# Kernel optimization log

Measured on AMD Instinct MI355X. Metric: run time of the kernel, lower is better.

Reference implementation:

```python
import jax, jax.numpy as jnp
import numpy as np
from jax import lax

HIDDEN = 1024
OUT = 768  # g_gpt_emb_dim (distilgpt2 n_embd)
BATCH = 512


def setup_inputs() -> dict:
    key = jax.random.key(0)
    ks = jax.random.split(key, 8)
    s_i = 1.0 / np.sqrt(HIDDEN)
    return {
        "src": jax.random.normal(ks[0], (1, BATCH, OUT), jnp.float32),
        "hidden": jax.random.normal(ks[1], (1, BATCH, HIDDEN), jnp.float32),
        "W_ih": jax.random.uniform(ks[2], (3 * HIDDEN, OUT), jnp.float32, -s_i, s_i),
        "W_hh": jax.random.uniform(ks[3], (3 * HIDDEN, HIDDEN), jnp.float32, -s_i, s_i),
        "b_ih": jax.random.uniform(ks[4], (3 * HIDDEN,), jnp.float32, -s_i, s_i),
        "b_hh": jax.random.uniform(ks[5], (3 * HIDDEN,), jnp.float32, -s_i, s_i),
        "fc_W": jax.random.uniform(ks[6], (OUT, 2 * HIDDEN), jnp.float32, -s_i, s_i),
        "fc_b": jax.random.uniform(ks[7], (OUT,), jnp.float32, -s_i, s_i),
        "output_len": 256,
    }


def reference(src, hidden, W_ih, W_hh, b_ih, b_hh, fc_W, fc_b, output_len):
    # src: [src_len, B, OUT]; hidden: [1, B, H]
    context = hidden[0]          # [B, H] (kept fixed across steps)
    h0 = hidden[0]               # [B, H] GRU state
    x0 = src[0]                  # [B, OUT] first decoder input

    def gru_cell(x, h):
        # PyTorch GRU cell: gates ordered (r, z, n)
        gi = x @ W_ih.T + b_ih   # [B, 3H]
        gh = h @ W_hh.T + b_hh   # [B, 3H]
        i_r, i_z, i_n = jnp.split(gi, 3, axis=-1)
        h_r, h_z, h_n = jnp.split(gh, 3, axis=-1)
        r = jax.nn.sigmoid(i_r + h_r)
        z = jax.nn.sigmoid(i_z + h_z)
        n = jnp.tanh(i_n + r * h_n)
        return (1.0 - z) * n + z * h

    def step(carry, _):
        h, x = carry
        h_new = gru_cell(x, h)                                   # [B, H]
        emb_con = jnp.concatenate([h_new, context], axis=-1)     # [B, 2H]
        fc_out = emb_con @ fc_W.T + fc_b                         # [B, OUT]
        return (h_new, fc_out), fc_out

    _, outputs = lax.scan(step, (h0, x0), None, length=output_len)
    return outputs  # [output_len, B, OUT]
```

## Files before the change

kernel.cpp:

```cpp
#include <hip/hip_runtime.h>

#define H    1024
#define OUTD 768
#define BSZ  512
#define TSTEPS 256
#define N3H  3072
#define NEXT 4864
#define TILE_E 4096
#define MT_E   65536
#define SLOT_E 524288

typedef __attribute__((ext_vector_type(8))) short bf16x8;
typedef __attribute__((ext_vector_type(4))) float f32x4;

__device__ __forceinline__ unsigned short f2bf(float f){
  unsigned u = __builtin_bit_cast(unsigned, f);
  u += 0x7fffu + ((u >> 16) & 1u);
  return (unsigned short)(u >> 16);
}
__device__ __forceinline__ float sigm(float x){ return 1.f/(1.f+__expf(-x)); }

__device__ __forceinline__ int swz_off(int r, int c){
  return (r<<6) | (((c>>3) ^ (r&7))<<3) | (c&7);
}

#define GLOAD16(gp, lp) __builtin_amdgcn_global_load_lds( \
    (__attribute__((address_space(1))) void*)(gp), \
    (__attribute__((address_space(3))) void*)(lp), 16, 0, 0)

__global__ void conv_bf(unsigned short* dst, const float* src, int n){
  int i = blockIdx.x*256 + threadIdx.x;
  if (i < n) dst[i] = f2bf(src[i]);
}
__global__ void conv_rows(unsigned short* dst, const float* src, int rows, int cols,
                          int sstride, int soff){
  int i = blockIdx.x*256 + threadIdx.x;
  if (i < rows*cols){ int r = i/cols, c = i - r*cols; dst[i] = f2bf(src[r*sstride + soff + c]); }
}
__global__ void transp_fcw(unsigned short* dst, const float* fcw){
  __shared__ float tile[64][65];
  int k0 = blockIdx.x*64, o0 = blockIdx.y*64;
  int t = threadIdx.x; int rr = t>>2, cs = (t&3)*16;
  for (int j=0;j<16;j++) tile[rr][cs+j] = fcw[(size_t)(o0+rr)*2048 + k0+cs+j];
  __syncthreads();
  for (int j=0;j<16;j++) dst[(size_t)(k0+rr)*768 + o0+cs+j] = f2bf(tile[cs+j][rr]);
}

__global__ void asm_wext(unsigned short* Wext, const float* Wcomb, const float* Whh,
                         const float* fcW){
  int idx = blockIdx.x*256 + threadIdx.x;
  if (idx >= NEXT*H) return;
  int n = idx >> 10, k = idx & 1023;
  float v;
  if (n < 4096){
    int c = (n>>4)&3, jj = ((n>>6)<<4) | (n&15);
    if (c==0)      v = Wcomb[(size_t)jj*H + k]       + Whh[(size_t)jj*H + k];
    else if (c==1) v = Wcomb[(size_t)(H+jj)*H + k]   + Whh[(size_t)(H+jj)*H + k];
    else if (c==2) v = Wcomb[(size_t)(2*H+jj)*H + k];
    else           v = Whh[(size_t)(2*H+jj)*H + k];
  } else {
    v = fcW[(size_t)(n-4096)*2048 + k];
  }
  Wext[(size_t)(n>>6)*MT_E + (k>>6)*TILE_E + swz_off(n&63, k&63)] = f2bf(v);
}

__global__ void asm_const(float* cst, const float* dmat, const float* fcctx,
                          const float* b_hh){
  int idx = blockIdx.x*256 + threadIdx.x;
  if (idx >= BSZ*NEXT) return;
  int b = idx / NEXT, n = idx - b*NEXT;
  float v;
  if (n < 4096){
    int c = (n>>4)&3, jj = ((n>>6)<<4) | (n&15);
    if (c==0)      v = dmat[(size_t)b*N3H + jj]       + b_hh[jj];
    else if (c==1) v = dmat[(size_t)b*N3H + H + jj]   + b_hh[H+jj];
    else if (c==2) v = dmat[(size_t)b*N3H + 2*H + jj];
    else           v = b_hh[2*H + jj];
  } else {
    v = fcctx[(size_t)b*OUTD + (n-4096)];
  }
  cst[idx] = v;
}

__global__ void gru0(const float* gi, const float* gh, const float* hidden,
                     unsigned short* hbf, float* hf){
  int idx = blockIdx.x*256 + threadIdx.x;
  if (idx >= BSZ*H) return;
  int b = idx >> 10, j = idx & 1023;
  float r  = sigm(gi[(size_t)b*N3H + j]       + gh[(size_t)b*N3H + j]);
  float z  = sigm(gi[(size_t)b*N3H + H + j]   + gh[(size_t)b*N3H + H + j]);
  float nn = tanhf(gi[(size_t)b*N3H + 2*H + j] + r*gh[(size_t)b*N3H + 2*H + j]);
  float ho = hidden[idx];
  float hn = nn + z*(ho - nn);
  hf[idx] = hn;
  hbf[(size_t)(b>>6)*MT_E + (j>>6)*TILE_E + swz_off(b&63, j&63)] = f2bf(hn);
}

__global__ __launch_bounds__(256) void gemm_bt(const unsigned short* __restrict__ A,
    const unsigned short* __restrict__ Bt, const float* __restrict__ bias,
    float* __restrict__ C, int N, int K){
  __shared__ unsigned short As[64][72];
  __shared__ unsigned short Bs[64][72];
  int tid = threadIdx.x, wave = tid>>6, lane = tid&63;
  int m0 = blockIdx.y*64, n0 = blockIdx.x*64;
  int lr = tid>>2, lc = (tid&3)*16;
  const unsigned short* Ag = A + (size_t)(m0+lr)*K + lc;
  const unsigned short* Bg = Bt + (size_t)(n0+lr)*K + lc;
  f32x4 acc[4];
  #pragma unroll
  for (int c=0;c<4;c++) acc[c] = (f32x4)0.f;
  int arow = wave*16 + (lane&15);
  int koff = (lane>>4)*8;
  for (int k0=0;k0<K;k0+=64){
    *(uint4*)&As[lr][lc]   = *(const uint4*)(Ag + k0);
    *(uint4*)&As[lr][lc+8] = *(const uint4*)(Ag + k0 + 8);
    *(uint4*)&Bs[lr][lc]   = *(const uint4*)(Bg + k0);
    *(uint4*)&Bs[lr][lc+8] = *(const uint4*)(Bg + k0 + 8);
    __syncthreads();
    #pragma unroll
    for (int kk=0;kk<2;kk++){
      bf16x8 af = *(const bf16x8*)&As[arow][kk*32 + koff];
      #pragma unroll
      for (int c=0;c<4;c++){
        bf16x8 bfr = *(const bf16x8*)&Bs[c*16 + (lane&15)][kk*32 + koff];
        acc[c] = __builtin_amdgcn_mfma_f32_16x16x32_bf16(af, bfr, acc[c], 0, 0, 0);
      }
    }
    __syncthreads();
  }
  int col = lane&15, rbase = m0 + wave*16 + (lane>>4)*4;
  #pragma unroll
  for (int c=0;c<4;c++){
    int n = n0 + c*16 + col;
    float bv = bias ? bias[n] : 0.f;
    #pragma unroll
    for (int i=0;i<4;i++) C[(size_t)(rbase+i)*N + n] = acc[c][i] + bv;
  }
}

__device__ __forceinline__ void mm64(const unsigned short* __restrict__ At,
                                     const unsigned short* __restrict__ Bt,
                                     unsigned short* sA, unsigned short* sB,
                                     f32x4 acc[4]){
  const int tid = threadIdx.x, wave = tid>>6, lane = tid&63;
  const int l8 = lane>>4, lx = lane&7;
  const int xg = ((l8 ^ lx) << 3);
  const int offA = ((wave<<4) | (lane&15))*64 + xg;
  const int offB = (lane&15)*64 + xg;
  const unsigned short* ga = At + (wave<<9) + (lane<<3);
  const unsigned short* gb = Bt + (wave<<9) + (lane<<3);
  unsigned short* lA = sA + (wave<<9);
  unsigned short* lB = sB + (wave<<9);
  GLOAD16(ga, lA); GLOAD16(ga+2048, lA+2048);
  GLOAD16(gb, lB); GLOAD16(gb+2048, lB+2048);
  __syncthreads();
  #pragma unroll 2
  for (int kt=0; kt<16; kt++){
    const int cb = kt & 1;
    if (kt < 15){
      const unsigned short* gan = ga + (kt+1)*TILE_E;
      const unsigned short* gbn = gb + (kt+1)*TILE_E;
      const int bo = (cb^1) << 12;
      GLOAD16(gan, lA+bo); GLOAD16(gan+2048, lA+bo+2048);
      GLOAD16(gbn, lB+bo); GLOAD16(gbn+2048, lB+bo+2048);
    }
    const unsigned short* A0 = sA + (cb<<12);
    const unsigned short* B0 = sB + (cb<<12);
    #pragma unroll
    for (int kk=0; kk<2; kk++){
      bf16x8 av = *(const bf16x8*)(A0 + (offA ^ (kk<<5)));
      #pragma unroll
      for (int c=0; c<4; c++){
        bf16x8 bv = *(const bf16x8*)(B0 + ((offB + (c<<10)) ^ (kk<<5)));
        acc[c] = __builtin_amdgcn_mfma_f32_16x16x32_bf16(av, bv, acc[c], 0, 0, 0);
      }
    }
    __syncthreads();
  }
}

__global__ __launch_bounds__(256) void gemm_rec(const unsigned short* __restrict__ hin,
    const float* __restrict__ hfin, const unsigned short* __restrict__ Wext,
    const float* __restrict__ cst, float* __restrict__ outp,
    unsigned short* __restrict__ hout, float* __restrict__ hfout){
  __shared__ __align__(16) unsigned short sA[2*4096];
  __shared__ __align__(16) unsigned short sB[2*4096];
  const int gx = gridDim.x;
  const int f = blockIdx.x + gx*blockIdx.y;
  const int q = f & 7, mm = f >> 3;
  const int v = q*gx + mm;
  const int bx = v >> 3, by = v & 7;
  f32x4 acc[4];
  #pragma unroll
  for (int c=0;c<4;c++) acc[c] = (f32x4)0.f;
  mm64(hin + (size_t)by*MT_E, Wext + (size_t)bx*MT_E, sA, sB, acc);
  const int tid = threadIdx.x, wave = tid>>6, lane = tid&63;
  const int col = lane & 15;
  const int rbase = by*64 + wave*16 + (lane>>4)*4;
  if (bx < 64){
    const int jj = bx*16 + col;
    const float* cbp = cst + bx*64 + col;
    const int tb = (jj>>6)*TILE_E;
    #pragma unroll
    for (int i=0;i<4;i++){
      const int b = rbase + i;
      const float* cr = cbp + (size_t)b*NEXT;
      float r  = sigm(acc[0][i] + cr[0]);
      float z  = sigm(acc[1][i] + cr[16]);
      float nn = tanhf((acc[2][i] + cr[32]) + r*(acc[3][i] + cr[48]));
      float hn = nn + z*(hfin[(size_t)b*H + jj] - nn);
      hfout[(size_t)b*H + jj] = hn;
      hout[(size_t)(b>>6)*MT_E + tb + swz_off(b&63, jj&63)] = f2bf(hn);
    }
  } else {
    const int o0 = (bx-64)*64;
    #pragma unroll
    for (int c=0;c<4;c++){
      const int oc = o0 + c*16 + col;
      #pragma unroll
      for (int i=0;i<4;i++){
        const int b = rbase + i;
        outp[(size_t)b*OUTD + oc] = acc[c][i] + cst[(size_t)b*NEXT + 4096 + oc];
      }
    }
  }
}

__global__ __launch_bounds__(256) void gemm_out(const unsigned short* __restrict__ hist,
    const unsigned short* __restrict__ Wext, const float* __restrict__ fcctx,
    float* __restrict__ outp){
  __shared__ __align__(16) unsigned short sA[2*4096];
  __shared__ __align__(16) unsigned short sB[2*4096];
  const int bx = blockIdx.x;
  const int g  = blockIdx.y;
  f32x4 acc[4];
  #pragma unroll
  for (int c=0;c<4;c++) acc[c] = (f32x4)0.f;
  mm64(hist + (size_t)g*MT_E, Wext + (size_t)(64+bx)*MT_E, sA, sB, acc);
  const int tid = threadIdx.x, wave = tid>>6, lane = tid&63;
  const int col = lane & 15;
  const int s = g>>3, mb = g&7;
  const int rb = mb*64 + wave*16 + (lane>>4)*4;
  float* outs = outp + (size_t)s*BSZ*OUTD;
  #pragma unroll
  for (int c=0;c<4;c++){
    const int oc = bx*64 + c*16 + col;
    #pragma unroll
    for (int i=0;i<4;i++){
      const int b = rb + i;
      outs[(size_t)b*OUTD + oc] = acc[c][i] + fcctx[(size_t)b*OUTD + oc];
    }
  }
}

extern "C" void kernel_launch(void* const* d_in, const int* in_sizes, int n_in,
                              void* d_out, int out_size, void* d_ws, size_t ws_size,
                              hipStream_t stream){
  const float* src    = (const float*)d_in[0];
  const float* hidden = (const float*)d_in[1];
  const float* W_ih   = (const float*)d_in[2];
  const float* W_hh   = (const float*)d_in[3];
  const float* b_ih   = (const float*)d_in[4];
  const float* b_hh   = (const float*)d_in[5];
  const float* fc_W   = (const float*)d_in[6];
  const float* fc_b   = (const float*)d_in[7];
  float* outp = (float*)d_out;

  char* p = (char*)d_ws;
  auto alloc = [&](size_t bytes){ char* r = p; p += (bytes + 255) & ~(size_t)255; return r; };
  unsigned short* Wih_bf   = (unsigned short*)alloc((size_t)N3H*OUTD*2);
  unsigned short* Whh_bf   = (unsigned short*)alloc((size_t)N3H*H*2);
  unsigned short* fcWbt    = (unsigned short*)alloc((size_t)OUTD*H*2);
  unsigned short* fcWT     = (unsigned short*)alloc((size_t)H*OUTD*2);
  unsigned short* ctx_bf   = (unsigned short*)alloc((size_t)BSZ*H*2);
  unsigned short* x0_bf    = (unsigned short*)alloc((size_t)BSZ*OUTD*2);
  float*          fcctx    = (float*)alloc((size_t)BSZ*OUTD*4);
  unsigned short* fcctx_bf = (unsigned short*)alloc((size_t)BSZ*OUTD*2);
  float*          Wcomb    = (float*)alloc((size_t)N3H*H*4);
  float*          dmat     = (float*)alloc((size_t)BSZ*N3H*4);
  unsigned short* Wext     = (unsigned short*)alloc((size_t)NEXT*H*2);
  float*          cst      = (float*)alloc((size_t)BSZ*NEXT*4);
  float*          gi       = (float*)alloc((size_t)BSZ*N3H*4);
  float*          gh       = (float*)alloc((size_t)BSZ*N3H*4);
  unsigned short* hbf      = (unsigned short*)alloc((size_t)2*BSZ*H*2);
  float*          hf       = (float*)alloc((size_t)2*BSZ*H*4);

  size_t used = (size_t)(p - (char*)d_ws);
  size_t hist_bytes = (size_t)TSTEPS*BSZ*H*2;
  bool defer = (used + hist_bytes + 4096) <= ws_size;
  unsigned short* hist = defer ? (unsigned short*)alloc(hist_bytes) : nullptr;

  auto cdiv = [](int a, int b){ return (a + b - 1)/b; };

  conv_bf<<<cdiv(N3H*OUTD,256),256,0,stream>>>(Wih_bf, W_ih, N3H*OUTD);
  conv_bf<<<cdiv(N3H*H,256),256,0,stream>>>(Whh_bf, W_hh, N3H*H);
  conv_bf<<<cdiv(BSZ*H,256),256,0,stream>>>(ctx_bf, hidden, BSZ*H);
  conv_bf<<<cdiv(BSZ*OUTD,256),256,0,stream>>>(x0_bf, src, BSZ*OUTD);
  conv_rows<<<cdiv(OUTD*H,256),256,0,stream>>>(fcWbt, fc_W, OUTD, H, 2*H, H);
  transp_fcw<<<dim3(16,12),256,0,stream>>>(fcWT, fc_W);

  gemm_bt<<<dim3(H/64, N3H/64),256,0,stream>>>(Wih_bf, fcWT, nullptr, Wcomb, H, OUTD);
  gemm_bt<<<dim3(OUTD/64, BSZ/64),256,0,stream>>>(ctx_bf, fcWbt, fc_b, fcctx, OUTD, H);
  conv_bf<<<cdiv(BSZ*OUTD,256),256,0,stream>>>(fcctx_bf, fcctx, BSZ*OUTD);
  gemm_bt<<<dim3(N3H/64, BSZ/64),256,0,stream>>>(fcctx_bf, Wih_bf, b_ih, dmat, N3H, OUTD);

  asm_wext<<<cdiv(NEXT*H,256),256,0,stream>>>(Wext, Wcomb, W_hh, fc_W);
  asm_const<<<cdiv(BSZ*NEXT,256),256,0,stream>>>(cst, dmat, fcctx, b_hh);

  gemm_bt<<<dim3(N3H/64, BSZ/64),256,0,stream>>>(x0_bf, Wih_bf, b_ih, gi, N3H, OUTD);
  gemm_bt<<<dim3(N3H/64, BSZ/64),256,0,stream>>>(ctx_bf, Whh_bf, b_hh, gh, N3H, H);

  if (defer){
    gru0<<<cdiv(BSZ*H,256),256,0,stream>>>(gi, gh, hidden, hist, hf + SLOT_E);
    for (int t=1; t<TSTEPS; t++){
      gemm_rec<<<dim3(64,8),256,0,stream>>>(
          hist + (size_t)(t-1)*SLOT_E, hf + (size_t)(t&1)*SLOT_E,
          Wext, cst, nullptr,
          hist + (size_t)t*SLOT_E, hf + (size_t)((t+1)&1)*SLOT_E);
    }
    gemm_out<<<dim3(12,2048),256,0,stream>>>(hist, Wext, fcctx, outp);
  } else {
    gru0<<<cdiv(BSZ*H,256),256,0,stream>>>(gi, gh, hidden, hbf + SLOT_E, hf + SLOT_E);
    for (int t=1; t<=TSTEPS; t++){
      gemm_rec<<<dim3(76,8),256,0,stream>>>(
          hbf + (size_t)(t&1)*SLOT_E, hf + (size_t)(t&1)*SLOT_E,
          Wext, cst, outp + (size_t)(t-1)*BSZ*OUTD,
          hbf + (size_t)((t+1)&1)*SLOT_E, hf + (size_t)((t+1)&1)*SLOT_E);
    }
  }
}
```

Baseline: 4.287 ms.

## Generalize MFMA GEMM core to larger register-blocked tiles with explicit waitcnt pipelining

Replaces the fixed 64x64 mm64 routine with a templated mmcore that gives each wave a 2x4 fragment block, so A fragments are reused across more MFMAs. The recurrent GEMM now covers 64x128 tiles with half the blocks, and the output GEMM uses 128x128 tiles with 512 threads. Staging is now two tiles ahead, governed by explicit s_waitcnt vmcnt and raw barriers in place of __syncthreads. This cuts LDS traffic per MFMA and barrier overhead. The cost is fewer blocks per recurrent step, meaning less parallelism across CUs, and more register pressure.

Result: faster. 3.839 ms (-10.5%).

```diff
diff --git a/kernel.cpp b/kernel.cpp
--- a/kernel.cpp
+++ b/kernel.cpp
@@ -27,6 +27,17 @@
 #define GLOAD16(gp, lp) __builtin_amdgcn_global_load_lds( \
     (__attribute__((address_space(1))) void*)(gp), \
     (__attribute__((address_space(3))) void*)(lp), 16, 0, 0)
+
+template<int N> __device__ __forceinline__ void waitv(){
+  if constexpr (N==0)      asm volatile("s_waitcnt vmcnt(0)" ::: "memory");
+  else if constexpr (N==4) asm volatile("s_waitcnt vmcnt(4)" ::: "memory");
+  else if constexpr (N==6) asm volatile("s_waitcnt vmcnt(6)" ::: "memory");
+  else if constexpr (N==8) asm volatile("s_waitcnt vmcnt(8)" ::: "memory");
+}
+__device__ __forceinline__ void waitlgkm0(){
+  asm volatile("s_waitcnt lgkmcnt(0)" ::: "memory");
+}
+__device__ __forceinline__ void bar(){ __builtin_amdgcn_s_barrier(); }
 
 __global__ void conv_bf(unsigned short* dst, const float* src, int n){
   int i = blockIdx.x*256 + threadIdx.x;
@@ -138,44 +149,84 @@
   }
 }
 
-__device__ __forceinline__ void mm64(const unsigned short* __restrict__ At,
-                                     const unsigned short* __restrict__ Bt,
-                                     unsigned short* sA, unsigned short* sB,
-                                     f32x4 acc[4]){
+template<int MT, int NT, int WAVES, int WM, int WN, int MF, int NF>
+__device__ __forceinline__ void mmcore(const unsigned short* __restrict__ Ag,
+                                       const unsigned short* __restrict__ Bg,
+                                       unsigned short* sbuf,
+                                       f32x4 (&acc)[MF][NF]){
+  constexpr int TT = MT + NT;
+  constexpr int L  = 8*TT/WAVES;
+  static_assert(8*TT == L*WAVES, "load split");
   const int tid = threadIdx.x, wave = tid>>6, lane = tid&63;
-  const int l8 = lane>>4, lx = lane&7;
-  const int xg = ((l8 ^ lx) << 3);
-  const int offA = ((wave<<4) | (lane&15))*64 + xg;
-  const int offB = (lane&15)*64 + xg;
-  const unsigned short* ga = At + (wave<<9) + (lane<<3);
-  const unsigned short* gb = Bt + (wave<<9) + (lane<<3);
-  unsigned short* lA = sA + (wave<<9);
-  unsigned short* lB = sB + (wave<<9);
-  GLOAD16(ga, lA); GLOAD16(ga+2048, lA+2048);
-  GLOAD16(gb, lB); GLOAD16(gb+2048, lB+2048);
-  __syncthreads();
-  #pragma unroll 2
+  const int wm = wave / WN, wn = wave % WN;
+  const int l8 = lane>>4, c15 = lane&15;
+
+  int abase[MF], axr[MF];
+  #pragma unroll
+  for (int f=0; f<MF; f++){
+    int row = wm*(MF*16) + f*16 + c15;
+    abase[f] = ((row>>6)*TILE_E) + ((row&63)<<6);
+    axr[f]   = row & 7;
+  }
+  int bbase[NF], bxr[NF];
+  #pragma unroll
+  for (int c=0; c<NF; c++){
+    int cc = wn*(NF*16) + c*16 + c15;
+    bbase[c] = ((MT + (cc>>6))*TILE_E) + ((cc&63)<<6);
+    bxr[c]   = cc & 7;
+  }
+
+  const unsigned short* gsrc[L];
+  unsigned short* ldst[L];
+  #pragma unroll
+  for (int i=0;i<L;i++){
+    int j = wave*L + i;
+    int tile = j>>3, sub = j&7;
+    const unsigned short* base = (tile < MT) ? (Ag + (size_t)tile*MT_E)
+                                             : (Bg + (size_t)(tile-MT)*MT_E);
+    gsrc[i] = base + sub*512 + lane*8;
+    ldst[i] = sbuf + tile*TILE_E + sub*512;
+  }
+  auto STG = [&](int kt, int b){
+    #pragma unroll
+    for (int i=0;i<L;i++)
+      GLOAD16(gsrc[i] + (size_t)kt*TILE_E, ldst[i] + b*(TT*TILE_E));
+  };
+
+  STG(0,0);
+  STG(1,1);
+  waitv<L>();
+  bar();
+
+  #pragma unroll
   for (int kt=0; kt<16; kt++){
     const int cb = kt & 1;
+    const unsigned short* B0 = sbuf + cb*(TT*TILE_E);
+    #pragma unroll
+    for (int kk=0; kk<2; kk++){
+      bf16x8 av[MF];
+      #pragma unroll
+      for (int f=0; f<MF; f++)
+        av[f] = *(const bf16x8*)(B0 + abase[f] + (((kk*4 + l8) ^ axr[f])<<3));
+      #pragma unroll
+      for (int c=0; c<NF; c++){
+        bf16x8 bv = *(const bf16x8*)(B0 + bbase[c] + (((kk*4 + l8) ^ bxr[c])<<3));
+        #pragma unroll
+        for (int f=0; f<MF; f++)
+          acc[f][c] = __builtin_amdgcn_mfma_f32_16x16x32_bf16(av[f], bv, acc[f][c], 0,0,0);
+      }
+    }
     if (kt < 15){
-      const unsigned short* gan = ga + (kt+1)*TILE_E;
-      const unsigned short* gbn = gb + (kt+1)*TILE_E;
-      const int bo = (cb^1) << 12;
-      GLOAD16(gan, lA+bo); GLOAD16(gan+2048, lA+bo+2048);
-      GLOAD16(gbn, lB+bo); GLOAD16(gbn+2048, lB+bo+2048);
-    }
-    const unsigned short* A0 = sA + (cb<<12);
-    const unsigned short* B0 = sB + (cb<<12);
-    #pragma unroll
-    for (int kk=0; kk<2; kk++){
-      bf16x8 av = *(const bf16x8*)(A0 + (offA ^ (kk<<5)));
-      #pragma unroll
-      for (int c=0; c<4; c++){
-        bf16x8 bv = *(const bf16x8*)(B0 + ((offB + (c<<10)) ^ (kk<<5)));
-        acc[c] = __builtin_amdgcn_mfma_f32_16x16x32_bf16(av, bv, acc[c], 0, 0, 0);
-      }
-    }
-    __syncthreads();
+      waitlgkm0();
+      bar();
+      if (kt < 14){
+        STG(kt+2, cb);
+        waitv<L>();
+      } else {
+        waitv<0>();
+      }
+      bar();
+    }
   }
 }
 
@@ -183,72 +234,78 @@
     const float* __restrict__ hfin, const unsigned short* __restrict__ Wext,
     const float* __restrict__ cst, float* __restrict__ outp,
     unsigned short* __restrict__ hout, float* __restrict__ hfout){
-  __shared__ __align__(16) unsigned short sA[2*4096];
-  __shared__ __align__(16) unsigned short sB[2*4096];
-  const int gx = gridDim.x;
-  const int f = blockIdx.x + gx*blockIdx.y;
-  const int q = f & 7, mm = f >> 3;
-  const int v = q*gx + mm;
-  const int bx = v >> 3, by = v & 7;
-  f32x4 acc[4];
-  #pragma unroll
-  for (int c=0;c<4;c++) acc[c] = (f32x4)0.f;
-  mm64(hin + (size_t)by*MT_E, Wext + (size_t)bx*MT_E, sA, sB, acc);
+  __shared__ __align__(16) unsigned short sbuf[2*3*TILE_E];
+  int bx, by;
+  if (gridDim.x == 32){
+    int f = blockIdx.x + 32*blockIdx.y;
+    int q = f & 7, mm = f >> 3;
+    bx = q*4 + (mm>>3); by = mm & 7;
+  } else { bx = blockIdx.x; by = blockIdx.y; }
+
+  f32x4 acc[2][4] = {};
+  mmcore<1,2,4,2,2,2,4>(hin + (size_t)by*MT_E, Wext + (size_t)(2*bx)*MT_E, sbuf, acc);
+
   const int tid = threadIdx.x, wave = tid>>6, lane = tid&63;
-  const int col = lane & 15;
-  const int rbase = by*64 + wave*16 + (lane>>4)*4;
-  if (bx < 64){
-    const int jj = bx*16 + col;
-    const float* cbp = cst + bx*64 + col;
+  const int wm = wave>>1, wn = wave&1, col = lane&15;
+  const int rb = by*64 + wm*32 + ((lane>>4)<<2);
+  if (bx < 32){
+    const int g  = bx*2 + wn;
+    const int jj = g*16 + col;
     const int tb = (jj>>6)*TILE_E;
     #pragma unroll
-    for (int i=0;i<4;i++){
-      const int b = rbase + i;
-      const float* cr = cbp + (size_t)b*NEXT;
-      float r  = sigm(acc[0][i] + cr[0]);
-      float z  = sigm(acc[1][i] + cr[16]);
-      float nn = tanhf((acc[2][i] + cr[32]) + r*(acc[3][i] + cr[48]));
-      float hn = nn + z*(hfin[(size_t)b*H + jj] - nn);
-      hfout[(size_t)b*H + jj] = hn;
-      hout[(size_t)(b>>6)*MT_E + tb + swz_off(b&63, jj&63)] = f2bf(hn);
+    for (int f=0; f<2; f++){
+      #pragma unroll
+      for (int i=0;i<4;i++){
+        int b = rb + f*16 + i;
+        const float* cr = cst + (size_t)b*NEXT + g*64 + col;
+        float r  = sigm(acc[f][0][i] + cr[0]);
+        float z  = sigm(acc[f][1][i] + cr[16]);
+        float nn = tanhf((acc[f][2][i] + cr[32]) + r*(acc[f][3][i] + cr[48]));
+        float hn = nn + z*(hfin[(size_t)b*H + jj] - nn);
+        hfout[(size_t)b*H + jj] = hn;
+        hout[(size_t)(b>>6)*MT_E + tb + swz_off(b&63, jj&63)] = f2bf(hn);
+      }
     }
   } else {
-    const int o0 = (bx-64)*64;
+    const int o0 = (bx-32)*128 + wn*64;
     #pragma unroll
     for (int c=0;c<4;c++){
-      const int oc = o0 + c*16 + col;
-      #pragma unroll
-      for (int i=0;i<4;i++){
-        const int b = rbase + i;
-        outp[(size_t)b*OUTD + oc] = acc[c][i] + cst[(size_t)b*NEXT + 4096 + oc];
-      }
-    }
-  }
-}
-
-__global__ __launch_bounds__(256) void gemm_out(const unsigned short* __restrict__ hist,
+      int oc = o0 + c*16 + col;
+      #pragma unroll
+      for (int f=0; f<2; f++){
+        #pragma unroll
+        for (int i=0;i<4;i++){
+          int b = rb + f*16 + i;
+          outp[(size_t)b*OUTD + oc] = acc[f][c][i] + cst[(size_t)b*NEXT + 4096 + oc];
+        }
+      }
+    }
+  }
+}
+
+__global__ __launch_bounds__(512, 4) void gemm_out(const unsigned short* __restrict__ hist,
     const unsigned short* __restrict__ Wext, const float* __restrict__ fcctx,
     float* __restrict__ outp){
-  __shared__ __align__(16) unsigned short sA[2*4096];
-  __shared__ __align__(16) unsigned short sB[2*4096];
+  __shared__ __align__(16) unsigned short sbuf[2*4*TILE_E];
   const int bx = blockIdx.x;
-  const int g  = blockIdx.y;
-  f32x4 acc[4];
-  #pragma unroll
-  for (int c=0;c<4;c++) acc[c] = (f32x4)0.f;
-  mm64(hist + (size_t)g*MT_E, Wext + (size_t)(64+bx)*MT_E, sA, sB, acc);
+  const int gy = blockIdx.y;
+  f32x4 acc[2][4] = {};
+  mmcore<2,2,8,4,2,2,4>(hist + (size_t)gy*2*MT_E, Wext + (size_t)(64 + 2*bx)*MT_E, sbuf, acc);
   const int tid = threadIdx.x, wave = tid>>6, lane = tid&63;
-  const int col = lane & 15;
-  const int s = g>>3, mb = g&7;
-  const int rb = mb*64 + wave*16 + (lane>>4)*4;
-  float* outs = outp + (size_t)s*BSZ*OUTD;
-  #pragma unroll
-  for (int c=0;c<4;c++){
-    const int oc = bx*64 + c*16 + col;
-    #pragma unroll
-    for (int i=0;i<4;i++){
-      const int b = rb + i;
-      outs[(size_t)b*OUTD + oc] = acc[c][i] + fcctx[(size_t)b*OUTD + oc];
+  const int wm = wave>>1, wn = wave&1, col = lane&15;
+  #pragma unroll
+  for (int f=0; f<2; f++){
+    #pragma unroll
+    for (int c=0; c<4; c++){
+      int oc = bx*128 + wn*64 + c*16 + col;
+      #pragma unroll
+      for (int i=0;i<4;i++){
+        int lr = wm*32 + f*16 + ((lane>>4)<<2) + i;
+        size_t grow = (size_t)gy*128 + lr;
+        size_t s = grow >> 9;
+        int b = (int)(grow & 511);
+        outp[(s*BSZ + b)*OUTD + oc] = acc[f][c][i] + fcctx[(size_t)b*OUTD + oc];
+      }
     }
   }
 }
@@ -313,16 +370,16 @@
   if (defer){
     gru0<<<cdiv(BSZ*H,256),256,0,stream>>>(gi, gh, hidden, hist, hf + SLOT_E);
     for (int t=1; t<TSTEPS; t++){
-      gemm_rec<<<dim3(64,8),256,0,stream>>>(
+      gemm_rec<<<dim3(32,8),256,0,stream>>>(
           hist + (size_t)(t-1)*SLOT_E, hf + (size_t)(t&1)*SLOT_E,
           Wext, cst, nullptr,
           hist + (size_t)t*SLOT_E, hf + (size_t)((t+1)&1)*SLOT_E);
     }
-    gemm_out<<<dim3(12,2048),256,0,stream>>>(hist, Wext, fcctx, outp);
+    gemm_out<<<dim3(6,1024),512,0,stream>>>(hist, Wext, fcctx, outp);
   } else {
     gru0<<<cdiv(BSZ*H,256),256,0,stream>>>(gi, gh, hidden, hbf + SLOT_E, hf + SLOT_E);
     for (int t=1; t<=TSTEPS; t++){
-      gemm_rec<<<dim3(76,8),256,0,stream>>>(
+      gemm_rec<<<dim3(38,8),256,0,stream>>>(
           hbf + (size_t)(t&1)*SLOT_E, hf + (size_t)(t&1)*SLOT_E,
           Wext, cst, outp + (size_t)(t-1)*BSZ*OUTD,
           hbf + (size_t)((t+1)&1)*SLOT_E, hf + (size_t)((t+1)&1)*SLOT_E);
```
